# Performance work log

Hardware: AMD Instinct MI355X
Metric: run time of the kernel (lower is better)

Reference implementation:

```python
import jax, jax.numpy as jnp
import numpy as np

B, C, X = 64, 2, 262144
H = 256          # hidden_dim
K = 8            # max_fronts
THR = 1e-06      # diff_threshold
LN_EPS = 1e-5


def _layernorm(x, g, b):
    mu = jnp.mean(x, axis=-1, keepdims=True)
    var = jnp.var(x, axis=-1, keepdims=True)
    return (x - mu) * jax.lax.rsqrt(var + LN_EPS) * g + b


def setup_inputs() -> dict:
    key = jax.random.key(0)
    ks = jax.random.split(key, 16)
    density = jax.random.normal(ks[0], (B, X), dtype=jnp.float32)
    coords = jnp.broadcast_to(jnp.linspace(0.0, 1.0, X, dtype=jnp.float32), (B, X))
    x = jnp.stack([density, coords], axis=1)  # (B, 2, X)

    def lin(k, fan_in, shape):
        return jax.random.normal(k, shape, dtype=jnp.float32) * (1.0 / np.sqrt(fan_in))

    inp = {
        "x": x,
        # input_proj: Linear(6, H) + LayerNorm(H)
        "w_in": lin(ks[1], 6, (6, H)),
        "b_in": jnp.zeros((H,), jnp.float32),
        "ln_in_g": jnp.ones((H,), jnp.float32),
        "ln_in_b": jnp.zeros((H,), jnp.float32),
        # 3 residual blocks, stacked on leading axis
        "rb_ln_g": jnp.ones((3, H), jnp.float32),
        "rb_ln_b": jnp.zeros((3, H), jnp.float32),
        "rb_w1": lin(ks[2], H, (3, H, 2 * H)),
        "rb_b1": jnp.zeros((3, 2 * H), jnp.float32),
        "rb_w2": lin(ks[3], 2 * H, (3, 2 * H, H)),
        "rb_b2": jnp.zeros((3, H), jnp.float32),
        # output head: LayerNorm(H) -> Linear(H, H//2) -> GELU -> Linear(H//2, 2)
        "out_ln_g": jnp.ones((H,), jnp.float32),
        "out_ln_b": jnp.zeros((H,), jnp.float32),
        "out_w1": lin(ks[4], H, (H, H // 2)),
        "out_b1": jnp.zeros((H // 2,), jnp.float32),
        "out_w2": lin(ks[5], H // 2, (H // 2, 2)),
        "out_b2": jnp.zeros((2,), jnp.float32),
    }
    return inp


def _speed_predictor(uL, uR, w_in, b_in, ln_in_g, ln_in_b,
                     rb_ln_g, rb_ln_b, rb_w1, rb_b1, rb_w2, rb_b2,
                     out_ln_g, out_ln_b, out_w1, out_b1, out_w2, out_b2):
    diff = uL - uR
    feats = jnp.stack([uL, uR, diff, jnp.abs(diff), (uL + uR) * 0.5,
                       jnp.sign(diff)], axis=-1)          # (B, K, 6)
    h = jax.nn.gelu(_layernorm(feats @ w_in + b_in, ln_in_g, ln_in_b),
                    approximate=False)                    # (B, K, H)
    for i in range(3):  # fixed small layer loop
        z = _layernorm(h, rb_ln_g[i], rb_ln_b[i])
        z = jax.nn.gelu(z @ rb_w1[i] + rb_b1[i], approximate=False)
        h = h + (z @ rb_w2[i] + rb_b2[i])
    z = _layernorm(h, out_ln_g, out_ln_b)
    z = jax.nn.gelu(z @ out_w1 + out_b1, approximate=False)
    return z @ out_w2 + out_b2                            # (B, K, 2)


def reference(x, w_in, b_in, ln_in_g, ln_in_b,
              rb_ln_g, rb_ln_b, rb_w1, rb_b1, rb_w2, rb_b2,
              out_ln_g, out_ln_b, out_w1, out_b1, out_w2, out_b2):
    density = x[:, 0, :]
    coords = x[:, -1, :]
    left_vals, right_vals = density[:, :-1], density[:, 1:]
    has_disc = jnp.abs(left_vals - right_vals) > THR       # (B, X-1)
    all_fc = (coords[:, :-1] + coords[:, 1:]) * 0.5        # (B, X-1)
    front_count = jnp.sum(has_disc, axis=-1)               # (B,)
    score = jnp.where(has_disc, all_fc, jnp.inf)
    # smallest-K coords -> top_k of negated score (K <= X-1 here)
    _, idx = jax.lax.top_k(-score, K)                      # (B, K)
    uL = jnp.take_along_axis(left_vals, idx, axis=-1)
    uR = jnp.take_along_axis(right_vals, idx, axis=-1)
    fc = jnp.take_along_axis(all_fc, idx, axis=-1)
    valid = jnp.take_along_axis(has_disc, idx, axis=-1).astype(x.dtype)
    speed = _speed_predictor(uL, uR, w_in, b_in, ln_in_g, ln_in_b,
                             rb_ln_g, rb_ln_b, rb_w1, rb_b1, rb_w2, rb_b2,
                             out_ln_g, out_ln_b, out_w1, out_b1, out_w2, out_b2)
    front_params = jnp.concatenate(
        [jnp.transpose(speed, (0, 2, 1)),                  # (B, 2, K)
         uL[:, None], uR[:, None], fc[:, None], valid[:, None]], axis=1)
    return front_params, front_count
```

## Files before the change

kernel.cpp:

```cpp
#include <hip/hip_runtime.h>
#include <hip/hip_bf16.h>
#include <math.h>

#define XN 262144
#define NPAIR (XN - 1)
#define BN 64
#define HD 256
#define KK 8
#define THRC 1e-6f

__device__ __forceinline__ float gelu_f(float x) {
    return 0.5f * x * (1.0f + erff(x * 0.70710678118654752440f));
}

__device__ __forceinline__ unsigned short f2bf(float f) {
    unsigned int x = __float_as_uint(f);
    unsigned int r = (x + 0x7fffu + ((x >> 16) & 1u)) >> 16;
    return (unsigned short)r;
}

__global__ __launch_bounds__(256) void convert_kernel(
    const float* __restrict__ rb_w1, const float* __restrict__ rb_w2,
    const float* __restrict__ out_w1, unsigned short* __restrict__ bw) {
    int t = blockIdx.x * 256 + threadIdx.x;
    const float* s;
    if (t < 49152) s = rb_w1 + (size_t)t * 8;
    else if (t < 98304) s = rb_w2 + (size_t)(t - 49152) * 8;
    else s = out_w1 + (size_t)(t - 98304) * 8;
    float4 a = *(const float4*)s;
    float4 b = *(const float4*)(s + 4);
    union { unsigned short u[8]; uint4 v; } r;
    r.u[0] = f2bf(a.x); r.u[1] = f2bf(a.y); r.u[2] = f2bf(a.z); r.u[3] = f2bf(a.w);
    r.u[4] = f2bf(b.x); r.u[5] = f2bf(b.y); r.u[6] = f2bf(b.z); r.u[7] = f2bf(b.w);
    *(uint4*)(bw + (size_t)t * 8) = r.v;
}

__global__ __launch_bounds__(256) void count_select_kernel(
    const float* __restrict__ x, float* __restrict__ out,
    float* __restrict__ ws_uLuR, int* __restrict__ ws_cnt) {
    __shared__ int sred[4];
    const int b = blockIdx.x >> 4;
    const int p = blockIdx.x & 15;
    const float* row = x + (size_t)b * 2 * XN;
    const int tid = threadIdx.x;
    const int lane = tid & 63, wave = tid >> 6;

    if (p == 0 && tid < 64) {
        const float* c = row + XN;
        int idxs[KK];
        float vflag[KK];
        int found = 0;
        for (int base = 0; base < NPAIR && found < KK; base += 64) {
            int i = base + lane;
            bool v = (i < NPAIR) && (fabsf(row[i] - row[i + 1]) > THRC);
            unsigned long long m = __ballot(v);
            while (m && found < KK) {
                int l = __ffsll(m) - 1;
                idxs[found] = base + l;
                vflag[found] = 1.0f;
                ++found;
                m &= (m - 1);
            }
        }
        if (found < KK) {
            for (int base = 0; base < NPAIR && found < KK; base += 64) {
                int i = base + lane;
                bool v = (i < NPAIR) && !(fabsf(row[i] - row[i + 1]) > THRC);
                unsigned long long m = __ballot(v);
                while (m && found < KK) {
                    int l = __ffsll(m) - 1;
                    idxs[found] = base + l;
                    vflag[found] = 0.0f;
                    ++found;
                    m &= (m - 1);
                }
            }
        }
        if (lane < KK) {
            int i = idxs[lane];
            float uL = row[i];
            float uR = row[i + 1];
            float fc = (c[i] + c[i + 1]) * 0.5f;
            float* o = out + b * 48;
            o[16 + lane] = uL;
            o[24 + lane] = uR;
            o[32 + lane] = fc;
            o[40 + lane] = vflag[lane];
            ws_uLuR[(b * KK + lane) * 2 + 0] = uL;
            ws_uLuR[(b * KK + lane) * 2 + 1] = uR;
        }
    }

    int cnt = 0;
    const int base0 = p * 16384;
#pragma unroll
    for (int it = 0; it < 16; ++it) {
        int e0 = base0 + ((it << 8) + tid) * 4;
        float4 f = *(const float4*)(row + e0);
        cnt += (fabsf(f.x - f.y) > THRC);
        cnt += (fabsf(f.y - f.z) > THRC);
        cnt += (fabsf(f.z - f.w) > THRC);
        if (e0 + 4 < XN) {
            float e = row[e0 + 4];
            cnt += (fabsf(f.w - e) > THRC);
        }
    }
#pragma unroll
    for (int off = 32; off > 0; off >>= 1) cnt += __shfl_down(cnt, off, 64);
    if (lane == 0) sred[wave] = cnt;
    __syncthreads();
    if (tid == 0) ws_cnt[blockIdx.x] = sred[0] + sred[1] + sred[2] + sred[3];
}


#define BF8_FMA(w, z)                                                        \
    do {                                                                     \
        float f0, f1;                                                        \
        f0 = __uint_as_float((w).x << 16);                                   \
        f1 = __uint_as_float((w).x & 0xffff0000u);                           \
        a0[0] = fmaf(f0, (z).x, a0[0]); a1[0] = fmaf(f0, (z).y, a1[0]);      \
        a0[1] = fmaf(f1, (z).x, a0[1]); a1[1] = fmaf(f1, (z).y, a1[1]);      \
        f0 = __uint_as_float((w).y << 16);                                   \
        f1 = __uint_as_float((w).y & 0xffff0000u);                           \
        a0[2] = fmaf(f0, (z).x, a0[2]); a1[2] = fmaf(f0, (z).y, a1[2]);      \
        a0[3] = fmaf(f1, (z).x, a0[3]); a1[3] = fmaf(f1, (z).y, a1[3]);      \
        f0 = __uint_as_float((w).z << 16);                                   \
        f1 = __uint_as_float((w).z & 0xffff0000u);                           \
        a0[4] = fmaf(f0, (z).x, a0[4]); a1[4] = fmaf(f0, (z).y, a1[4]);      \
        a0[5] = fmaf(f1, (z).x, a0[5]); a1[5] = fmaf(f1, (z).y, a1[5]);      \
        f0 = __uint_as_float((w).w << 16);                                   \
        f1 = __uint_as_float((w).w & 0xffff0000u);                           \
        a0[6] = fmaf(f0, (z).x, a0[6]); a1[6] = fmaf(f0, (z).y, a1[6]);      \
        a0[7] = fmaf(f1, (z).x, a0[7]); a1[7] = fmaf(f1, (z).y, a1[7]);      \
    } while (0)

__global__ __launch_bounds__(512) void mlp_kernel(
    const float* __restrict__ ws_uLuR, const int* __restrict__ ws_cnt,
    const unsigned short* __restrict__ bw,
    const float* __restrict__ w_in, const float* __restrict__ b_in,
    const float* __restrict__ ln_in_g, const float* __restrict__ ln_in_b,
    const float* __restrict__ rb_ln_g, const float* __restrict__ rb_ln_b,
    const float* __restrict__ rb_b1, const float* __restrict__ rb_b2,
    const float* __restrict__ out_ln_g, const float* __restrict__ out_ln_b,
    const float* __restrict__ out_b1,
    const float* __restrict__ out_w2, const float* __restrict__ out_b2,
    float* __restrict__ out) {
    __shared__ float2 hsv[HD];
    __shared__ float2 ztv[HD];
    __shared__ float2 z2tv[2 * HD];
    __shared__ float2 z3tv[HD / 2];
    __shared__ float part[8192];
    __shared__ float red[8][2][2];
    __shared__ float stat[2][2];
    __shared__ float fin[2][4];

    const int tid = threadIdx.x;
    const int bid = blockIdx.x;
    const int b = bid >> 2;
    const int sub = bid & 3;
    const int wave = tid >> 6, lane = tid & 63;

    if (sub == 0 && wave == 0) {
        int v = (lane < 16) ? ws_cnt[b * 16 + lane] : 0;
#pragma unroll
        for (int off = 8; off > 0; off >>= 1) v += __shfl_down(v, off, 64);
        if (lane == 0) out[3072 + b] = (float)v;
    }

    if (tid < HD) {
        const int c = tid;
        float fw[6];
#pragma unroll
        for (int f = 0; f < 6; ++f) fw[f] = w_in[f * HD + c];
        float bin = b_in[c];
        float2 hv;
        float* hvp = (float*)&hv;
#pragma unroll
        for (int j = 0; j < 2; ++j) {
            int tok = b * KK + sub * 2 + j;
            float uL = ws_uLuR[tok * 2 + 0];
            float uR = ws_uLuR[tok * 2 + 1];
            float dd = uL - uR;
            float sg = (dd > 0.0f) ? 1.0f : ((dd < 0.0f) ? -1.0f : 0.0f);
            hvp[j] = bin + uL * fw[0] + uR * fw[1] + dd * fw[2] +
                     fabsf(dd) * fw[3] + (uL + uR) * 0.5f * fw[4] + sg * fw[5];
        }
        hsv[c] = hv;
    }
    __syncthreads();

#define LN_STATS()                                                            \
    do {                                                                      \
        if (tid < HD) {                                                       \
            float2 h2 = hsv[tid];                                             \
            float s[2] = {h2.x, h2.y};                                        \
            float q[2] = {h2.x * h2.x, h2.y * h2.y};                          \
            for (int off = 32; off > 0; off >>= 1) {                          \
                _Pragma("unroll") for (int j = 0; j < 2; ++j) {               \
                    s[j] += __shfl_down(s[j], off, 64);                       \
                    q[j] += __shfl_down(q[j], off, 64);                       \
                }                                                             \
            }                                                                 \
            if (lane == 0) {                                                  \
                _Pragma("unroll") for (int j = 0; j < 2; ++j) {               \
                    red[wave][j][0] = s[j];                                   \
                    red[wave][j][1] = q[j];                                   \
                }                                                             \
            }                                                                 \
        }                                                                     \
        __syncthreads();                                                      \
        if (tid < 2) {                                                        \
            float ts = 0.0f, tq = 0.0f;                                       \
            _Pragma("unroll") for (int w = 0; w < 4; ++w) {                   \
                ts += red[w][tid][0];                                         \
                tq += red[w][tid][1];                                         \
            }                                                                 \
            float mu = ts * (1.0f / 256.0f);                                  \
            float vr = tq * (1.0f / 256.0f) - mu * mu;                        \
            stat[tid][0] = mu;                                                \
            stat[tid][1] = rsqrtf(vr + 1e-5f);                                \
        }                                                                     \
        __syncthreads();                                                      \
    } while (0)

    LN_STATS();
    if (tid < HD) {
        const int c = tid;
        float g = ln_in_g[c], be = ln_in_b[c];
        float2 hv = hsv[c];
        hv.x = gelu_f((hv.x - stat[0][0]) * stat[0][1] * g + be);
        hv.y = gelu_f((hv.y - stat[1][0]) * stat[1][1] * g + be);
        hsv[c] = hv;
    }
    __syncthreads();

    for (int i = 0; i < 3; ++i) {
        LN_STATS();
        if (tid < HD) {
            const int c = tid;
            float gg = rb_ln_g[i * HD + c], bb = rb_ln_b[i * HD + c];
            float2 hv = hsv[c], zv;
            zv.x = (hv.x - stat[0][0]) * stat[0][1] * gg + bb;
            zv.y = (hv.y - stat[1][0]) * stat[1][1] * gg + bb;
            ztv[c] = zv;
        }
        __syncthreads();

        {
            const unsigned short* w1 = bw + (size_t)i * (HD * 2 * HD);
            const int cg = tid & 63, kh = tid >> 6;
            const unsigned short* wp = w1 + (size_t)(kh * 32) * (2 * HD) + cg * 8;
            float a0[8] = {0, 0, 0, 0, 0, 0, 0, 0};
            float a1[8] = {0, 0, 0, 0, 0, 0, 0, 0};
#pragma unroll 8
            for (int k = 0; k < 32; ++k) {
                uint4 w = *(const uint4*)wp;
                wp += 2 * HD;
                float2 z = ztv[kh * 32 + k];
                BF8_FMA(w, z);
            }
            float* pp = part + (kh * 64 + cg) * 16;
#pragma unroll
            for (int u = 0; u < 8; ++u) {
                pp[u * 2] = a0[u];
                pp[u * 2 + 1] = a1[u];
            }
        }
        __syncthreads();
        {
            const int c2 = tid;
            const int cg = c2 >> 3, u = c2 & 7;
            float vx = rb_b1[i * 2 * HD + c2];
            float vy = vx;
#pragma unroll
            for (int kh = 0; kh < 8; ++kh) {
                const float* pp = part + (kh * 64 + cg) * 16 + u * 2;
                vx += pp[0];
                vy += pp[1];
            }
            float2 zv;
            zv.x = gelu_f(vx);
            zv.y = gelu_f(vy);
            z2tv[c2] = zv;
        }
        __syncthreads();

        {
            const unsigned short* w2 = bw + 393216 + (size_t)i * (2 * HD * HD);
            const int cg2 = tid & 31, kh2 = tid >> 5;
            const unsigned short* wp = w2 + (size_t)(kh2 * 32) * HD + cg2 * 8;
            float a0[8] = {0, 0, 0, 0, 0, 0, 0, 0};
            float a1[8] = {0, 0, 0, 0, 0, 0, 0, 0};
#pragma unroll 8
            for (int k = 0; k < 32; ++k) {
                uint4 w = *(const uint4*)wp;
                wp += HD;
                float2 z = z2tv[kh2 * 32 + k];
                BF8_FMA(w, z);
            }
            float* pp = part + (kh2 * 32 + cg2) * 16;
#pragma unroll
            for (int u = 0; u < 8; ++u) {
                pp[u * 2] = a0[u];
                pp[u * 2 + 1] = a1[u];
            }
        }
        __syncthreads();
        if (tid < HD) {
            const int cg2 = tid >> 3, u = tid & 7;
            float vx = rb_b2[i * HD + tid];
            float vy = vx;
#pragma unroll
            for (int kh = 0; kh < 16; ++kh) {
                const float* pp = part + (kh * 32 + cg2) * 16 + u * 2;
                vx += pp[0];
                vy += pp[1];
            }
            float2 hv = hsv[tid];
            hv.x += vx;
            hv.y += vy;
            hsv[tid] = hv;
        }
        __syncthreads();
    }

    LN_STATS();
    if (tid < HD) {
        const int c = tid;
        float gg = out_ln_g[c], bb = out_ln_b[c];
        float2 hv = hsv[c], zv;
        zv.x = (hv.x - stat[0][0]) * stat[0][1] * gg + bb;
        zv.y = (hv.y - stat[1][0]) * stat[1][1] * gg + bb;
        ztv[c] = zv;
    }
    __syncthreads();

    {
        const unsigned short* ow1 = bw + 786432;
        const int cg3 = tid & 15, kh3 = tid >> 4;
        const unsigned short* wp = ow1 + (size_t)(kh3 * 8) * (HD / 2) + cg3 * 8;
        float a0[8] = {0, 0, 0, 0, 0, 0, 0, 0};
        float a1[8] = {0, 0, 0, 0, 0, 0, 0, 0};
#pragma unroll
        for (int k = 0; k < 8; ++k) {
            uint4 w = *(const uint4*)wp;
            wp += HD / 2;
            float2 z = ztv[kh3 * 8 + k];
            BF8_FMA(w, z);
        }
        float* pp = part + (kh3 * 16 + cg3) * 16;
#pragma unroll
        for (int u = 0; u < 8; ++u) {
            pp[u * 2] = a0[u];
            pp[u * 2 + 1] = a1[u];
        }
    }
    __syncthreads();
    if (tid < HD / 2) {
        const int cg3 = tid >> 3, u = tid & 7;
        float vx = out_b1[tid];
        float vy = vx;
#pragma unroll
        for (int kh = 0; kh < 32; ++kh) {
            const float* pp = part + (kh * 16 + cg3) * 16 + u * 2;
            vx += pp[0];
            vy += pp[1];
        }
        float2 zv;
        zv.x = gelu_f(vx);
        zv.y = gelu_f(vy);
        z3tv[tid] = zv;
    }
    __syncthreads();

    if (tid < HD / 2) {
        float2 z = z3tv[tid];
        float w0 = out_w2[tid * 2 + 0];
        float w1v = out_w2[tid * 2 + 1];
        float p[4];
        p[0] = z.x * w0; p[1] = z.x * w1v;
        p[2] = z.y * w0; p[3] = z.y * w1v;
#pragma unroll
        for (int off = 32; off > 0; off >>= 1) {
#pragma unroll
            for (int u = 0; u < 4; ++u) p[u] += __shfl_down(p[u], off, 64);
        }
        if (lane == 0) {
#pragma unroll
            for (int u = 0; u < 4; ++u) fin[wave][u] = p[u];
        }
    }
    __syncthreads();
    if (tid < 4) {
        int j = tid >> 1;
        int o = tid & 1;
        float s = out_b2[o] + fin[0][tid] + fin[1][tid];
        out[b * 48 + o * 8 + sub * 2 + j] = s;
    }
}

extern "C" void kernel_launch(void* const* d_in, const int* in_sizes, int n_in,
                              void* d_out, int out_size, void* d_ws, size_t ws_size,
                              hipStream_t stream) {
    const float* x        = (const float*)d_in[0];
    const float* w_in     = (const float*)d_in[1];
    const float* b_in     = (const float*)d_in[2];
    const float* ln_in_g  = (const float*)d_in[3];
    const float* ln_in_b  = (const float*)d_in[4];
    const float* rb_ln_g  = (const float*)d_in[5];
    const float* rb_ln_b  = (const float*)d_in[6];
    const float* rb_w1    = (const float*)d_in[7];
    const float* rb_b1    = (const float*)d_in[8];
    const float* rb_w2    = (const float*)d_in[9];
    const float* rb_b2    = (const float*)d_in[10];
    const float* out_ln_g = (const float*)d_in[11];
    const float* out_ln_b = (const float*)d_in[12];
    const float* out_w1   = (const float*)d_in[13];
    const float* out_b1   = (const float*)d_in[14];
    const float* out_w2   = (const float*)d_in[15];
    const float* out_b2   = (const float*)d_in[16];

    float* out = (float*)d_out;
    float* wsf = (float*)d_ws;
    int* wsc = (int*)(wsf + 1024);
    unsigned short* bw = (unsigned short*)(wsf + 2048);

    convert_kernel<<<400, 256, 0, stream>>>(rb_w1, rb_w2, out_w1, bw);
    count_select_kernel<<<BN * 16, 256, 0, stream>>>(x, out, wsf, wsc);
    mlp_kernel<<<BN * 4, 512, 0, stream>>>(
        wsf, wsc, bw, w_in, b_in, ln_in_g, ln_in_b, rb_ln_g, rb_ln_b,
        rb_b1, rb_b2, out_ln_g, out_ln_b, out_b1, out_w2, out_b2, out);
}
```

Before: 245.7 us.

## Fuse count/select into MLP kernel with atomic front counts

Merges the counting/selection kernel and the MLP kernel into one launch. The first 512 blocks count discontinuities and atomically add per-row totals into the output, which is zeroed by a memset. The remaining blocks each redo the front selection scan themselves and pass uL/uR through shared memory instead of a workspace. This removes one kernel launch and its dependency gap, so the count pass can overlap the MLP. In exchange the selection scan is repeated four times per row, and float atomics plus an extra memset are added.

```diff
diff --git a/kernel.cpp b/kernel.cpp
--- a/kernel.cpp
+++ b/kernel.cpp
@@ -34,84 +34,6 @@
     r.u[4] = f2bf(b.x); r.u[5] = f2bf(b.y); r.u[6] = f2bf(b.z); r.u[7] = f2bf(b.w);
     *(uint4*)(bw + (size_t)t * 8) = r.v;
 }
-
-__global__ __launch_bounds__(256) void count_select_kernel(
-    const float* __restrict__ x, float* __restrict__ out,
-    float* __restrict__ ws_uLuR, int* __restrict__ ws_cnt) {
-    __shared__ int sred[4];
-    const int b = blockIdx.x >> 4;
-    const int p = blockIdx.x & 15;
-    const float* row = x + (size_t)b * 2 * XN;
-    const int tid = threadIdx.x;
-    const int lane = tid & 63, wave = tid >> 6;
-
-    if (p == 0 && tid < 64) {
-        const float* c = row + XN;
-        int idxs[KK];
-        float vflag[KK];
-        int found = 0;
-        for (int base = 0; base < NPAIR && found < KK; base += 64) {
-            int i = base + lane;
-            bool v = (i < NPAIR) && (fabsf(row[i] - row[i + 1]) > THRC);
-            unsigned long long m = __ballot(v);
-            while (m && found < KK) {
-                int l = __ffsll(m) - 1;
-                idxs[found] = base + l;
-                vflag[found] = 1.0f;
-                ++found;
-                m &= (m - 1);
-            }
-        }
-        if (found < KK) {
-            for (int base = 0; base < NPAIR && found < KK; base += 64) {
-                int i = base + lane;
-                bool v = (i < NPAIR) && !(fabsf(row[i] - row[i + 1]) > THRC);
-                unsigned long long m = __ballot(v);
-                while (m && found < KK) {
-                    int l = __ffsll(m) - 1;
-                    idxs[found] = base + l;
-                    vflag[found] = 0.0f;
-                    ++found;
-                    m &= (m - 1);
-                }
-            }
-        }
-        if (lane < KK) {
-            int i = idxs[lane];
-            float uL = row[i];
-            float uR = row[i + 1];
-            float fc = (c[i] + c[i + 1]) * 0.5f;
-            float* o = out + b * 48;
-            o[16 + lane] = uL;
-            o[24 + lane] = uR;
-            o[32 + lane] = fc;
-            o[40 + lane] = vflag[lane];
-            ws_uLuR[(b * KK + lane) * 2 + 0] = uL;
-            ws_uLuR[(b * KK + lane) * 2 + 1] = uR;
-        }
-    }
-
-    int cnt = 0;
-    const int base0 = p * 16384;
-#pragma unroll
-    for (int it = 0; it < 16; ++it) {
-        int e0 = base0 + ((it << 8) + tid) * 4;
-        float4 f = *(const float4*)(row + e0);
-        cnt += (fabsf(f.x - f.y) > THRC);
-        cnt += (fabsf(f.y - f.z) > THRC);
-        cnt += (fabsf(f.z - f.w) > THRC);
-        if (e0 + 4 < XN) {
-            float e = row[e0 + 4];
-            cnt += (fabsf(f.w - e) > THRC);
-        }
-    }
-#pragma unroll
-    for (int off = 32; off > 0; off >>= 1) cnt += __shfl_down(cnt, off, 64);
-    if (lane == 0) sred[wave] = cnt;
-    __syncthreads();
-    if (tid == 0) ws_cnt[blockIdx.x] = sred[0] + sred[1] + sred[2] + sred[3];
-}
-
 
 #define BF8_FMA(w, z)                                                        \
     do {                                                                     \
@@ -134,9 +56,8 @@
         a0[7] = fmaf(f1, (z).x, a0[7]); a1[7] = fmaf(f1, (z).y, a1[7]);      \
     } while (0)
 
-__global__ __launch_bounds__(512) void mlp_kernel(
-    const float* __restrict__ ws_uLuR, const int* __restrict__ ws_cnt,
-    const unsigned short* __restrict__ bw,
+__global__ __launch_bounds__(512) void fused_kernel(
+    const float* __restrict__ x, const unsigned short* __restrict__ bw,
     const float* __restrict__ w_in, const float* __restrict__ b_in,
     const float* __restrict__ ln_in_g, const float* __restrict__ ln_in_b,
     const float* __restrict__ rb_ln_g, const float* __restrict__ rb_ln_b,
@@ -153,19 +74,100 @@
     __shared__ float red[8][2][2];
     __shared__ float stat[2][2];
     __shared__ float fin[2][4];
-
+    __shared__ float2 suv[2];
+    __shared__ int sred[8];
+
+    const int blk = blockIdx.x;
     const int tid = threadIdx.x;
-    const int bid = blockIdx.x;
-    const int b = bid >> 2;
-    const int sub = bid & 3;
-    const int wave = tid >> 6, lane = tid & 63;
-
-    if (sub == 0 && wave == 0) {
-        int v = (lane < 16) ? ws_cnt[b * 16 + lane] : 0;
-#pragma unroll
-        for (int off = 8; off > 0; off >>= 1) v += __shfl_down(v, off, 64);
-        if (lane == 0) out[3072 + b] = (float)v;
-    }
+    const int lane = tid & 63, wave = tid >> 6;
+
+    if (blk < 512) {
+        const int b = blk >> 3;
+        const int s = blk & 7;
+        const float* row = x + (size_t)b * 2 * XN;
+        int cnt = 0;
+        const int base0 = s * 32768;
+#pragma unroll
+        for (int it = 0; it < 16; ++it) {
+            int e0 = base0 + ((it << 9) + tid) * 4;
+            float4 f = *(const float4*)(row + e0);
+            cnt += (fabsf(f.x - f.y) > THRC);
+            cnt += (fabsf(f.y - f.z) > THRC);
+            cnt += (fabsf(f.z - f.w) > THRC);
+            if (e0 + 4 < XN) {
+                float e = row[e0 + 4];
+                cnt += (fabsf(f.w - e) > THRC);
+            }
+        }
+#pragma unroll
+        for (int off = 32; off > 0; off >>= 1) cnt += __shfl_down(cnt, off, 64);
+        if (lane == 0) sred[wave] = cnt;
+        __syncthreads();
+        if (tid == 0) {
+            int t = 0;
+#pragma unroll
+            for (int w = 0; w < 8; ++w) t += sred[w];
+            atomicAdd(&out[3072 + b], (float)t);
+        }
+        return;
+    }
+
+    const int mb = blk - 512;
+    const int b = mb >> 2;
+    const int sub = mb & 3;
+    const float* row = x + (size_t)b * 2 * XN;
+
+    if (wave == 0) {
+        const float* c = row + XN;
+        int idxs[KK];
+        float vflag[KK];
+        int found = 0;
+        for (int base = 0; base < NPAIR && found < KK; base += 64) {
+            int i = base + lane;
+            bool v = (i < NPAIR) && (fabsf(row[i] - row[i + 1]) > THRC);
+            unsigned long long m = __ballot(v);
+            while (m && found < KK) {
+                int l = __ffsll(m) - 1;
+                idxs[found] = base + l;
+                vflag[found] = 1.0f;
+                ++found;
+                m &= (m - 1);
+            }
+        }
+        if (found < KK) {
+            for (int base = 0; base < NPAIR && found < KK; base += 64) {
+                int i = base + lane;
+                bool v = (i < NPAIR) && !(fabsf(row[i] - row[i + 1]) > THRC);
+                unsigned long long m = __ballot(v);
+                while (m && found < KK) {
+                    int l = __ffsll(m) - 1;
+                    idxs[found] = base + l;
+                    vflag[found] = 0.0f;
+                    ++found;
+                    m &= (m - 1);
+                }
+            }
+        }
+        if (lane < 2) {
+            int i = idxs[sub * 2 + lane];
+            float2 uv;
+            uv.x = row[i];
+            uv.y = row[i + 1];
+            suv[lane] = uv;
+        }
+        if (sub == 0 && lane < KK) {
+            int i = idxs[lane];
+            float uL = row[i];
+            float uR = row[i + 1];
+            float fc = (c[i] + c[i + 1]) * 0.5f;
+            float* o = out + b * 48;
+            o[16 + lane] = uL;
+            o[24 + lane] = uR;
+            o[32 + lane] = fc;
+            o[40 + lane] = vflag[lane];
+        }
+    }
+    __syncthreads();
 
     if (tid < HD) {
         const int c = tid;
@@ -177,9 +179,8 @@
         float* hvp = (float*)&hv;
 #pragma unroll
         for (int j = 0; j < 2; ++j) {
-            int tok = b * KK + sub * 2 + j;
-            float uL = ws_uLuR[tok * 2 + 0];
-            float uR = ws_uLuR[tok * 2 + 1];
+            float uL = suv[j].x;
+            float uR = suv[j].y;
             float dd = uL - uR;
             float sg = (dd > 0.0f) ? 1.0f : ((dd < 0.0f) ? -1.0f : 0.0f);
             hvp[j] = bin + uL * fw[0] + uR * fw[1] + dd * fw[2] +
@@ -421,13 +422,11 @@
     const float* out_b2   = (const float*)d_in[16];
 
     float* out = (float*)d_out;
-    float* wsf = (float*)d_ws;
-    int* wsc = (int*)(wsf + 1024);
-    unsigned short* bw = (unsigned short*)(wsf + 2048);
+    unsigned short* bw = (unsigned short*)d_ws;
 
     convert_kernel<<<400, 256, 0, stream>>>(rb_w1, rb_w2, out_w1, bw);
-    count_select_kernel<<<BN * 16, 256, 0, stream>>>(x, out, wsf, wsc);
-    mlp_kernel<<<BN * 4, 512, 0, stream>>>(
-        wsf, wsc, bw, w_in, b_in, ln_in_g, ln_in_b, rb_ln_g, rb_ln_b,
+    hipMemsetAsync(out + 3072, 0, BN * sizeof(float), stream);
+    fused_kernel<<<768, 512, 0, stream>>>(
+        x, bw, w_in, b_in, ln_in_g, ln_in_b, rb_ln_g, rb_ln_b,
         rb_b1, rb_b2, out_ln_g, out_ln_b, out_b1, out_w2, out_b2, out);
 }
```

New measurement: 250.4 us. Within noise of the previous version (+1.9%).

## Repack MLP weights per-column and prefetch next layer into registers

Applied to the files above, without the earlier changes.

The bf16 conversion kernel now writes the residual and output-head weights in a column-major, 8-row-chunked layout, so each thread owns one (or a half-K slice of one) output column. Weights for the next matmul are prefetched into a 32-entry uint4 register array before the barrier, overlapping global loads with LN and GELU work. The large shared-memory partial-sum buffer and its 8/16/32-way reductions give way to small 2-way or 4-way combines. The cost is higher register pressure (128 VGPRs for the prefetch array) at 512 threads per block, which may limit occupancy or cause spills.

```diff
diff --git a/kernel.cpp b/kernel.cpp
--- a/kernel.cpp
+++ b/kernel.cpp
@@ -24,15 +24,33 @@
     const float* __restrict__ out_w1, unsigned short* __restrict__ bw) {
     int t = blockIdx.x * 256 + threadIdx.x;
     const float* s;
-    if (t < 49152) s = rb_w1 + (size_t)t * 8;
-    else if (t < 98304) s = rb_w2 + (size_t)(t - 49152) * 8;
-    else s = out_w1 + (size_t)(t - 98304) * 8;
-    float4 a = *(const float4*)s;
-    float4 b = *(const float4*)(s + 4);
-    union { unsigned short u[8]; uint4 v; } r;
-    r.u[0] = f2bf(a.x); r.u[1] = f2bf(a.y); r.u[2] = f2bf(a.z); r.u[3] = f2bf(a.w);
-    r.u[4] = f2bf(b.x); r.u[5] = f2bf(b.y); r.u[6] = f2bf(b.z); r.u[7] = f2bf(b.w);
-    *(uint4*)(bw + (size_t)t * 8) = r.v;
+    int stride;
+    unsigned short* d;
+    if (t < 49152) {
+        int i = t / 16384, r = t % 16384;
+        int c = r >> 9, n = r & 511;
+        s = rb_w1 + (size_t)i * 131072 + (size_t)c * 8 * 512 + n;
+        stride = 512;
+        d = bw + (size_t)i * 131072 + (((n >> 6) * 32 + c) * 512 + (n & 63) * 8);
+    } else if (t < 98304) {
+        int t2 = t - 49152;
+        int i = t2 / 16384, r = t2 % 16384;
+        int c = r >> 8, n = r & 255;
+        s = rb_w2 + (size_t)i * 131072 + (size_t)c * 8 * 256 + n;
+        stride = 256;
+        d = bw + 393216 + (size_t)i * 131072 +
+            (((n >> 6) * 64 + c) * 512 + (n & 63) * 8);
+    } else {
+        int r = t - 98304;
+        int c = r >> 7, n = r & 127;
+        s = out_w1 + (size_t)c * 8 * 128 + n;
+        stride = 128;
+        d = bw + 786432 + (((n >> 6) * 32 + c) * 512 + (n & 63) * 8);
+    }
+    union { unsigned short u[8]; uint4 v; } rr;
+#pragma unroll
+    for (int j = 0; j < 8; ++j) rr.u[j] = f2bf(s[j * stride]);
+    *(uint4*)d = rr.v;
 }
 
 __global__ __launch_bounds__(256) void count_select_kernel(
@@ -113,25 +131,25 @@
 }
 
 
-#define BF8_FMA(w, z)                                                        \
+#define DOT8(w, zq)                                                          \
     do {                                                                     \
-        float f0, f1;                                                        \
-        f0 = __uint_as_float((w).x << 16);                                   \
-        f1 = __uint_as_float((w).x & 0xffff0000u);                           \
-        a0[0] = fmaf(f0, (z).x, a0[0]); a1[0] = fmaf(f0, (z).y, a1[0]);      \
-        a0[1] = fmaf(f1, (z).x, a0[1]); a1[1] = fmaf(f1, (z).y, a1[1]);      \
-        f0 = __uint_as_float((w).y << 16);                                   \
-        f1 = __uint_as_float((w).y & 0xffff0000u);                           \
-        a0[2] = fmaf(f0, (z).x, a0[2]); a1[2] = fmaf(f0, (z).y, a1[2]);      \
-        a0[3] = fmaf(f1, (z).x, a0[3]); a1[3] = fmaf(f1, (z).y, a1[3]);      \
-        f0 = __uint_as_float((w).z << 16);                                   \
-        f1 = __uint_as_float((w).z & 0xffff0000u);                           \
-        a0[4] = fmaf(f0, (z).x, a0[4]); a1[4] = fmaf(f0, (z).y, a1[4]);      \
-        a0[5] = fmaf(f1, (z).x, a0[5]); a1[5] = fmaf(f1, (z).y, a1[5]);      \
-        f0 = __uint_as_float((w).w << 16);                                   \
-        f1 = __uint_as_float((w).w & 0xffff0000u);                           \
-        a0[6] = fmaf(f0, (z).x, a0[6]); a1[6] = fmaf(f0, (z).y, a1[6]);      \
-        a0[7] = fmaf(f1, (z).x, a0[7]); a1[7] = fmaf(f1, (z).y, a1[7]);      \
+        float4 q; unsigned int wu; float f0, f1;                             \
+        q = (zq)[0]; wu = (w).x;                                             \
+        f0 = __uint_as_float(wu << 16); f1 = __uint_as_float(wu & 0xffff0000u);\
+        ax0 = fmaf(f0, q.x, ax0); ay0 = fmaf(f0, q.y, ay0);                  \
+        ax1 = fmaf(f1, q.z, ax1); ay1 = fmaf(f1, q.w, ay1);                  \
+        q = (zq)[1]; wu = (w).y;                                             \
+        f0 = __uint_as_float(wu << 16); f1 = __uint_as_float(wu & 0xffff0000u);\
+        ax0 = fmaf(f0, q.x, ax0); ay0 = fmaf(f0, q.y, ay0);                  \
+        ax1 = fmaf(f1, q.z, ax1); ay1 = fmaf(f1, q.w, ay1);                  \
+        q = (zq)[2]; wu = (w).z;                                             \
+        f0 = __uint_as_float(wu << 16); f1 = __uint_as_float(wu & 0xffff0000u);\
+        ax0 = fmaf(f0, q.x, ax0); ay0 = fmaf(f0, q.y, ay0);                  \
+        ax1 = fmaf(f1, q.z, ax1); ay1 = fmaf(f1, q.w, ay1);                  \
+        q = (zq)[3]; wu = (w).w;                                             \
+        f0 = __uint_as_float(wu << 16); f1 = __uint_as_float(wu & 0xffff0000u);\
+        ax0 = fmaf(f0, q.x, ax0); ay0 = fmaf(f0, q.y, ay0);                  \
+        ax1 = fmaf(f1, q.z, ax1); ay1 = fmaf(f1, q.w, ay1);                  \
     } while (0)
 
 __global__ __launch_bounds__(512) void mlp_kernel(
@@ -149,7 +167,8 @@
     __shared__ float2 ztv[HD];
     __shared__ float2 z2tv[2 * HD];
     __shared__ float2 z3tv[HD / 2];
-    __shared__ float part[8192];
+    __shared__ float2 part2[2 * HD];
+    __shared__ float2 part3[4 * (HD/2)];
     __shared__ float red[8][2][2];
     __shared__ float stat[2][2];
     __shared__ float fin[2][4];
@@ -186,6 +205,14 @@
                      fabsf(dd) * fw[3] + (uL + uR) * 0.5f * fw[4] + sg * fw[5];
         }
         hsv[c] = hv;
+    }
+
+    uint4 wr[32];
+    {
+        const unsigned short* wp =
+            bw + (((tid >> 6) * 32) * 512 + (tid & 63) * 8);
+#pragma unroll
+        for (int c = 0; c < 32; ++c) wr[c] = *(const uint4*)(wp + c * 512);
     }
     __syncthreads();
 
@@ -247,78 +274,63 @@
         __syncthreads();
 
         {
-            const unsigned short* w1 = bw + (size_t)i * (HD * 2 * HD);
-            const int cg = tid & 63, kh = tid >> 6;
-            const unsigned short* wp = w1 + (size_t)(kh * 32) * (2 * HD) + cg * 8;
-            float a0[8] = {0, 0, 0, 0, 0, 0, 0, 0};
-            float a1[8] = {0, 0, 0, 0, 0, 0, 0, 0};
-#pragma unroll 8
-            for (int k = 0; k < 32; ++k) {
-                uint4 w = *(const uint4*)wp;
-                wp += 2 * HD;
-                float2 z = ztv[kh * 32 + k];
-                BF8_FMA(w, z);
+            float ax0 = 0, ax1 = 0, ay0 = 0, ay1 = 0;
+            const float* zb = (const float*)ztv;
+#pragma unroll
+            for (int c = 0; c < 32; ++c) {
+                uint4 w = wr[c];
+                const float4* zq = (const float4*)(zb + c * 16);
+                DOT8(w, zq);
             }
-            float* pp = part + (kh * 64 + cg) * 16;
-#pragma unroll
-            for (int u = 0; u < 8; ++u) {
-                pp[u * 2] = a0[u];
-                pp[u * 2 + 1] = a1[u];
+            float b1v = rb_b1[i * 2 * HD + tid];
+            float2 zv;
+            zv.x = gelu_f(ax0 + ax1 + b1v);
+            zv.y = gelu_f(ay0 + ay1 + b1v);
+            z2tv[tid] = zv;
+        }
+        {
+            const int col = tid & 255, kh = tid >> 8;
+            const unsigned short* wp = bw + 393216 + (size_t)i * 131072 +
+                (((col >> 6) * 64 + kh * 32) * 512 + (col & 63) * 8);
+#pragma unroll
+            for (int c = 0; c < 32; ++c) wr[c] = *(const uint4*)(wp + c * 512);
+        }
+        __syncthreads();
+
+        {
+            const int kh = tid >> 8;
+            float ax0 = 0, ax1 = 0, ay0 = 0, ay1 = 0;
+            const float* zb = (const float*)(z2tv + kh * 256);
+#pragma unroll
+            for (int c = 0; c < 32; ++c) {
+                uint4 w = wr[c];
+                const float4* zq = (const float4*)(zb + c * 16);
+                DOT8(w, zq);
             }
-        }
-        __syncthreads();
-        {
-            const int c2 = tid;
-            const int cg = c2 >> 3, u = c2 & 7;
-            float vx = rb_b1[i * 2 * HD + c2];
-            float vy = vx;
-#pragma unroll
-            for (int kh = 0; kh < 8; ++kh) {
-                const float* pp = part + (kh * 64 + cg) * 16 + u * 2;
-                vx += pp[0];
-                vy += pp[1];
-            }
-            float2 zv;
-            zv.x = gelu_f(vx);
-            zv.y = gelu_f(vy);
-            z2tv[c2] = zv;
-        }
-        __syncthreads();
-
-        {
-            const unsigned short* w2 = bw + 393216 + (size_t)i * (2 * HD * HD);
-            const int cg2 = tid & 31, kh2 = tid >> 5;
-            const unsigned short* wp = w2 + (size_t)(kh2 * 32) * HD + cg2 * 8;
-            float a0[8] = {0, 0, 0, 0, 0, 0, 0, 0};
-            float a1[8] = {0, 0, 0, 0, 0, 0, 0, 0};
-#pragma unroll 8
-            for (int k = 0; k < 32; ++k) {
-                uint4 w = *(const uint4*)wp;
-                wp += HD;
-                float2 z = z2tv[kh2 * 32 + k];
-                BF8_FMA(w, z);
-            }
-            float* pp = part + (kh2 * 32 + cg2) * 16;
-#pragma unroll
-            for (int u = 0; u < 8; ++u) {
-                pp[u * 2] = a0[u];
-                pp[u * 2 + 1] = a1[u];
-            }
+            float2 pv;
+            pv.x = ax0 + ax1;
+            pv.y = ay0 + ay1;
+            part2[tid] = pv;
+        }
+        if (i < 2) {
+            const unsigned short* wp = bw + (size_t)(i + 1) * 131072 +
+                (((tid >> 6) * 32) * 512 + (tid & 63) * 8);
+#pragma unroll
+            for (int c = 0; c < 32; ++c) wr[c] = *(const uint4*)(wp + c * 512);
+        } else {
+            const int col = tid & 127, kq = tid >> 7;
+            const unsigned short* wp = bw + 786432 +
+                (((col >> 6) * 32 + kq * 8) * 512 + (col & 63) * 8);
+#pragma unroll
+            for (int c = 0; c < 8; ++c) wr[c] = *(const uint4*)(wp + c * 512);
         }
         __syncthreads();
         if (tid < HD) {
-            const int cg2 = tid >> 3, u = tid & 7;
-            float vx = rb_b2[i * HD + tid];
-            float vy = vx;
-#pragma unroll
-            for (int kh = 0; kh < 16; ++kh) {
-                const float* pp = part + (kh * 32 + cg2) * 16 + u * 2;
-                vx += pp[0];
-                vy += pp[1];
-            }
+            float2 p0 = part2[tid], p1 = part2[HD + tid];
+            float bb = rb_b2[i * HD + tid];
             float2 hv = hsv[tid];
-            hv.x += vx;
-            hv.y += vy;
+            hv.x += p0.x + p1.x + bb;
+            hv.y += p0.y + p1.y + bb;
             hsv[tid] = hv;
         }
         __syncthreads();
@@ -336,39 +348,28 @@
     __syncthreads();
 
     {
-        const unsigned short* ow1 = bw + 786432;
-        const int cg3 = tid & 15, kh3 = tid >> 4;
-        const unsigned short* wp = ow1 + (size_t)(kh3 * 8) * (HD / 2) + cg3 * 8;
-        float a0[8] = {0, 0, 0, 0, 0, 0, 0, 0};
-        float a1[8] = {0, 0, 0, 0, 0, 0, 0, 0};
-#pragma unroll
-        for (int k = 0; k < 8; ++k) {
-            uint4 w = *(const uint4*)wp;
-            wp += HD / 2;
-            float2 z = ztv[kh3 * 8 + k];
-            BF8_FMA(w, z);
-        }
-        float* pp = part + (kh3 * 16 + cg3) * 16;
-#pragma unroll
-        for (int u = 0; u < 8; ++u) {
-            pp[u * 2] = a0[u];
-            pp[u * 2 + 1] = a1[u];
-        }
+        const int kq = tid >> 7;
+        float ax0 = 0, ax1 = 0, ay0 = 0, ay1 = 0;
+        const float* zb = (const float*)(ztv + kq * 64);
+#pragma unroll
+        for (int c = 0; c < 8; ++c) {
+            uint4 w = wr[c];
+            const float4* zq = (const float4*)(zb + c * 16);
+            DOT8(w, zq);
+        }
+        float2 pv;
+        pv.x = ax0 + ax1;
+        pv.y = ay0 + ay1;
+        part3[tid] = pv;
     }
     __syncthreads();
     if (tid < HD / 2) {
-        const int cg3 = tid >> 3, u = tid & 7;
-        float vx = out_b1[tid];
-        float vy = vx;
-#pragma unroll
-        for (int kh = 0; kh < 32; ++kh) {
-            const float* pp = part + (kh * 16 + cg3) * 16 + u * 2;
-            vx += pp[0];
-            vy += pp[1];
-        }
+        float2 p0 = part3[tid], p1 = part3[128 + tid];
+        float2 p2 = part3[256 + tid], p3 = part3[384 + tid];
+        float bv = out_b1[tid];
         float2 zv;
-        zv.x = gelu_f(vx);
-        zv.y = gelu_f(vy);
+        zv.x = gelu_f(p0.x + p1.x + p2.x + p3.x + bv);
+        zv.y = gelu_f(p0.y + p1.y + p2.y + p3.y + bv);
         z3tv[tid] = zv;
     }
     __syncthreads();
```

After: 684.2 us. 178% more time.
